# Kernel optimization log

Hardware: AMD Instinct MI355X
Metric: run time of the kernel (lower is better)

Reference implementation:

```python
import jax, jax.numpy as jnp
import numpy as np

N = 100000
F_IN = 128
HID = 16
C = 16
E = 3200000


def setup_inputs() -> dict:
    key = jax.random.key(0)
    k1, k2, k3, k4, k5, k6 = jax.random.split(key, 6)
    x = jax.random.normal(k1, (N, F_IN), dtype=jnp.float32)
    edge_index = jax.random.randint(k2, (2, E), 0, N, dtype=jnp.int64)
    # GCNConv weight (glorot) + bias
    W1 = jax.random.normal(k3, (F_IN, HID), dtype=jnp.float32) * (1.0 / np.sqrt(F_IN))
    b1 = jnp.zeros((HID,), dtype=jnp.float32)
    # pooling linear
    Wp = jax.random.normal(k4, (HID, C), dtype=jnp.float32) * (1.0 / np.sqrt(HID))
    bp = jax.random.normal(k5, (C,), dtype=jnp.float32) * 0.01
    return {"x": x, "W1": W1, "b1": b1, "Wp": Wp, "bp": bp, "edge_index": edge_index}


def gcn_conv(x, W, b, edge_index, num_nodes):
    # PyG GCNConv: add self-loops, symmetric normalization D^-1/2 (A+I) D^-1/2
    loop = jnp.arange(num_nodes, dtype=edge_index.dtype)
    src = jnp.concatenate([edge_index[0], loop])
    dst = jnp.concatenate([edge_index[1], loop])
    ones = jnp.ones_like(dst, dtype=x.dtype)
    deg = jax.ops.segment_sum(ones, dst, num_segments=num_nodes)  # [N]
    dinv = jnp.where(deg > 0, jax.lax.rsqrt(deg), 0.0)
    norm = dinv[src] * dinv[dst]  # [E+N]
    h = x @ W  # [N, HID] transform before aggregation (fewer bytes moved)
    msgs = h[src] * norm[:, None]  # gather + scale
    agg = jax.ops.segment_sum(msgs, dst, num_segments=num_nodes)  # scatter-add
    return agg + b


def reference(x, W1, b1, Wp, bp, edge_index):
    h = jax.nn.relu(gcn_conv(x, W1, b1, edge_index, N))  # [N, HID]
    s = jax.nn.softmax(h @ Wp + bp, axis=1)  # [N, C]
    return s
```

## Files before the change

### kernel.cpp

```cpp
#include <hip/hip_runtime.h>


#define PCHUNK 4096
#define SPLITS 4
#define ACH 2048

__device__ __forceinline__ float bf2f(unsigned int u16) {
    return __uint_as_float(u16 << 16);
}
__device__ __forceinline__ unsigned short f2bf(float f) {
    unsigned int u = __float_as_uint(f);
    u += 0x7fffu + ((u >> 16) & 1u);
    return (unsigned short)(u >> 16);
}

__device__ __forceinline__ void atomAddF(float* p, float v) {
    unsafeAtomicAdd(p, v);
}

__device__ __forceinline__ int voteBf16(const unsigned int* xw, int tid, int* scratch) {
    if (tid == 0) *scratch = 0;
    __syncthreads();
    unsigned int w = xw[tid];
    unsigned int lo = w & 0xffffu;
    unsigned int elo = (lo >> 7) & 0xffu;
    if (lo == 0u || (elo >= 100u && elo <= 140u)) atomicAdd(scratch, 1);
    __syncthreads();
    return (*scratch >= 160) ? 1 : 0;
}

__global__ __launch_bounds__(256) void k_part(const int* __restrict__ ei,
                                              int* __restrict__ cursor,
                                              unsigned int* __restrict__ bkt,
                                              int E, int Nn, int NB, int cap) {
    __shared__ int lhist[512];
    __shared__ int lexcl[512];
    __shared__ int lbase[512];
    __shared__ int sa[512], sb[512];
    __shared__ unsigned int stage[PCHUNK];
    __shared__ ushort sbk[PCHUNK];
    __shared__ int stot_s;
    __shared__ int v64_s;
    int tid = threadIdx.x;
    lhist[tid] = 0; lhist[tid + 256] = 0;
    if (tid == 0) v64_s = 0;
    __syncthreads();
    if (((const unsigned int*)ei)[2 * tid + 1] != 0u) atomicAdd(&v64_s, 1);
    __syncthreads();
    int is64 = (v64_s == 0) ? 1 : 0;
    int e0 = blockIdx.x * PCHUNK;
    int ss[16], dd[16];
    #pragma unroll
    for (int i = 0; i < 16; ++i) {
        int e = e0 + i * 256 + tid;
        int s = -1, d = -1;
        if (e < E) {
            if (is64) { s = ei[2 * e]; d = ei[2 * (E + e)]; }
            else      { s = ei[e];     d = ei[E + e]; }
            if ((unsigned)s >= (unsigned)Nn || (unsigned)d >= (unsigned)Nn) { s = -1; d = -1; }
        }
        ss[i] = s; dd[i] = d;
        if (d >= 0) atomicAdd(&lhist[d >> 8], 1);
    }
    __syncthreads();
    sa[tid] = lhist[tid]; sa[tid + 256] = lhist[tid + 256];
    __syncthreads();
    int* cur = sa; int* nxt = sb;
    for (int off = 1; off < 512; off <<= 1) {
        nxt[tid] = cur[tid] + ((tid >= off) ? cur[tid - off] : 0);
        int t2 = tid + 256;
        nxt[t2] = cur[t2] + ((t2 >= off) ? cur[t2 - off] : 0);
        __syncthreads();
        int* t = cur; cur = nxt; nxt = t;
    }
    lexcl[tid] = cur[tid] - lhist[tid];
    lexcl[tid + 256] = cur[tid + 256] - lhist[tid + 256];
    if (tid == 0) stot_s = cur[511];
    __syncthreads();
    for (int b = tid; b < 512; b += 256) {
        int c = lhist[b];
        if (b < NB && c > 0) {
            int base = atomicAdd(&cursor[b], c);
            lbase[b] = b * cap + base - lexcl[b];
        } else lbase[b] = 0;
        lhist[b] = lexcl[b];
    }
    __syncthreads();
    #pragma unroll
    for (int i = 0; i < 16; ++i) {
        if (dd[i] >= 0) {
            int b = dd[i] >> 8;
            int q = atomicAdd(&lhist[b], 1);
            stage[q] = (unsigned)ss[i] | ((unsigned)(dd[i] & 255) << 17);
            sbk[q] = (ushort)b;
        }
    }
    __syncthreads();
    int stot = stot_s;
    for (int q = tid; q < stot; q += 256) {
        int b = sbk[q];
        int pos = lbase[b] + q;
        if (pos < (b + 1) * cap) bkt[pos] = stage[q];
    }
}

__global__ __launch_bounds__(256) void k_gemmD(const void* __restrict__ xraw,
                                               const void* __restrict__ w1raw,
                                               const unsigned int* __restrict__ bkt,
                                               const int* __restrict__ cursor,
                                               float* __restrict__ dinv,
                                               ushort* __restrict__ hs16,
                                               float* __restrict__ agg,
                                               int Nn, int cap) {
    __shared__ float sWt[16 * 132];
    __shared__ int ldeg[256];
    __shared__ float sdv[256];
    __shared__ int vote_s;
    const ushort* xb = (const ushort*)xraw;
    const float* xf = (const float*)xraw;
    int tid = threadIdx.x, b = blockIdx.x;
    const int isbf = voteBf16((const unsigned int*)xraw, tid, &vote_s);
    ldeg[tid] = 0;
    if (isbf) {
        const ushort* w1 = (const ushort*)w1raw;
        for (int i = tid; i < 2048; i += 256) {
            int k = i >> 4, j = i & 15;
            sWt[j * 132 + k] = bf2f(w1[i]);
        }
    } else {
        const float* w1 = (const float*)w1raw;
        for (int i = tid; i < 2048; i += 256) {
            int k = i >> 4, j = i & 15;
            sWt[j * 132 + k] = w1[i];
        }
    }
    __syncthreads();
    int len = min(cursor[b], cap);
    int bb = b * cap;
    for (int e = tid; e < len; e += 256)
        atomicAdd(&ldeg[(bkt[bb + e] >> 17) & 255u], 1);
    __syncthreads();
    {
        float dv = rsqrtf((float)(ldeg[tid] + 1));
        sdv[tid] = dv;
        int n = (b << 8) + tid;
        if (n < Nn) dinv[n] = dv;
    }
    __syncthreads();
    int hq = tid & 3;
    int nodeq = tid >> 2;
    int n0 = (b << 8) + nodeq * 4;
    float acc[4][4] = {};
    for (int ko = 0; ko < 16; ++ko) {
        float xv[4][8];
        #pragma unroll
        for (int r = 0; r < 4; ++r) {
            int n = n0 + r;
            if (n < Nn) {
                if (isbf) {
                    uint4 q = *reinterpret_cast<const uint4*>(xb + (size_t)n * 128 + ko * 8);
                    xv[r][0] = bf2f(q.x & 0xffffu); xv[r][1] = bf2f(q.x >> 16);
                    xv[r][2] = bf2f(q.y & 0xffffu); xv[r][3] = bf2f(q.y >> 16);
                    xv[r][4] = bf2f(q.z & 0xffffu); xv[r][5] = bf2f(q.z >> 16);
                    xv[r][6] = bf2f(q.w & 0xffffu); xv[r][7] = bf2f(q.w >> 16);
                } else {
                    const float4* p = reinterpret_cast<const float4*>(xf + (size_t)n * 128 + ko * 8);
                    float4 a = p[0], bf = p[1];
                    xv[r][0] = a.x; xv[r][1] = a.y; xv[r][2] = a.z; xv[r][3] = a.w;
                    xv[r][4] = bf.x; xv[r][5] = bf.y; xv[r][6] = bf.z; xv[r][7] = bf.w;
                }
            } else {
                #pragma unroll
                for (int u = 0; u < 8; ++u) xv[r][u] = 0.f;
            }
        }
        #pragma unroll
        for (int c = 0; c < 4; ++c) {
            const float* wr = &sWt[(hq * 4 + c) * 132 + ko * 8];
            float4 w0 = *reinterpret_cast<const float4*>(wr);
            float4 w1v = *reinterpret_cast<const float4*>(wr + 4);
            #pragma unroll
            for (int r = 0; r < 4; ++r) {
                acc[r][c] += xv[r][0] * w0.x + xv[r][1] * w0.y + xv[r][2] * w0.z + xv[r][3] * w0.w
                           + xv[r][4] * w1v.x + xv[r][5] * w1v.y + xv[r][6] * w1v.z + xv[r][7] * w1v.w;
            }
        }
    }
    #pragma unroll
    for (int r = 0; r < 4; ++r) {
        int n = n0 + r;
        if (n < Nn) {
            float dv = sdv[nodeq * 4 + r];
            float4 o = make_float4(acc[r][0] * dv, acc[r][1] * dv, acc[r][2] * dv, acc[r][3] * dv);
            ushort4 o16;
            o16.x = f2bf(o.x); o16.y = f2bf(o.y); o16.z = f2bf(o.z); o16.w = f2bf(o.w);
            *reinterpret_cast<ushort4*>(hs16 + (size_t)n * 16 + hq * 4) = o16;
            *reinterpret_cast<float4*>(agg + (size_t)n * 16 + hq * 4) = o;
        }
    }
}

__global__ __launch_bounds__(256) void k_aggS(const unsigned int* __restrict__ bkt,
                                              const int* __restrict__ cursor,
                                              const ushort* __restrict__ hs16,
                                              float* __restrict__ agg, int Nn, int cap) {
    __shared__ unsigned int sSorted[ACH];
    __shared__ int cnt[256], excl[256];
    __shared__ int sc[2][256];
    __shared__ int tot_s;
    int tid = threadIdx.x;
    int b = blockIdx.x >> 2, sp = blockIdx.x & 3;
    int len = min(cursor[b], cap);
    int bb = b * cap;
    int s0 = (int)(((long long)len * sp) >> 2);
    int s1 = (int)(((long long)len * (sp + 1)) >> 2);
    int g = tid >> 4, j = tid & 15;
    float racc[16] = {};
    for (int c0 = s0; c0 < s1; c0 += ACH) {
        cnt[tid] = 0;
        __syncthreads();
        unsigned ue[8];
        #pragma unroll
        for (int i = 0; i < 8; ++i) {
            int idx = c0 + i * 256 + tid;
            if (idx < s1) {
                ue[i] = bkt[bb + idx];
                atomicAdd(&cnt[(ue[i] >> 17) & 255u], 1);
            } else ue[i] = 0xffffffffu;
        }
        __syncthreads();
        int v = cnt[tid];
        sc[0][tid] = v;
        __syncthreads();
        int pi = 0;
        for (int off = 1; off < 256; off <<= 1) {
            sc[pi ^ 1][tid] = sc[pi][tid] + ((tid >= off) ? sc[pi][tid - off] : 0);
            __syncthreads();
            pi ^= 1;
        }
        int ex = sc[pi][tid] - v;
        excl[tid] = ex;
        cnt[tid] = ex;
        if (tid == 255) tot_s = sc[pi][255];
        __syncthreads();
        #pragma unroll
        for (int i = 0; i < 8; ++i) {
            if (ue[i] != 0xffffffffu) {
                int q = atomicAdd(&cnt[(ue[i] >> 17) & 255u], 1);
                sSorted[q] = ue[i];
            }
        }
        __syncthreads();
        int tot = tot_s;
        #pragma unroll
        for (int nn = 0; nn < 16; ++nn) {
            int node = g * 16 + nn;
            int segS = excl[node];
            int segE = (node == 255) ? tot : excl[node + 1];
            float acc = 0.f;
            #pragma unroll 1
            for (int base = segS; base < segE; base += 16) {
                int m = segE - base;
                unsigned e16[16];
                float vv[16];
                #pragma unroll
                for (int i = 0; i < 16; ++i) {
                    int idx = base + i;
                    e16[i] = sSorted[(idx < segE) ? idx : segS];
                }
                #pragma unroll
                for (int i = 0; i < 16; ++i)
                    vv[i] = bf2f(hs16[(size_t)(e16[i] & 0x1ffffu) * 16 + j]);
                #pragma unroll
                for (int i = 0; i < 16; ++i)
                    vv[i] = (i < m) ? vv[i] : 0.f;
                #pragma unroll
                for (int off = 8; off >= 1; off >>= 1) {
                    #pragma unroll
                    for (int i = 0; i < off; ++i) vv[i] += vv[i + off];
                }
                acc += vv[0];
            }
            racc[nn] += acc;
        }
        __syncthreads();
    }
    int nbase = b << 8;
    #pragma unroll
    for (int nn = 0; nn < 16; ++nn) {
        int n = nbase + g * 16 + nn;
        float v = racc[nn];
        bool nz = (n < Nn) && (v != 0.f);
        if (__any(nz)) {
            if (n < Nn) atomAddF(&agg[(size_t)n * 16 + j], v);
        }
    }
}

__global__ __launch_bounds__(256) void k_final(const float* __restrict__ agg,
                                               const float* __restrict__ dinv,
                                               const void* __restrict__ xraw,
                                               const void* __restrict__ b1raw,
                                               const void* __restrict__ wpraw,
                                               const void* __restrict__ bpraw,
                                               void* __restrict__ outraw, int Nn) {
    __shared__ float sWp[256];
    __shared__ float sA[256];
    __shared__ int vote_s;
    int tid = threadIdx.x;
    const int isbf = voteBf16((const unsigned int*)xraw, tid, &vote_s);
    sWp[tid] = isbf ? bf2f(((const ushort*)wpraw)[tid]) : ((const float*)wpraw)[tid];
    int nl = tid >> 4, c = tid & 15;
    float b1v = isbf ? bf2f(((const ushort*)b1raw)[c]) : ((const float*)b1raw)[c];
    float bpv = isbf ? bf2f(((const ushort*)bpraw)[c]) : ((const float*)bpraw)[c];
    int base0 = blockIdx.x * 64;
    #pragma unroll 1
    for (int pass = 0; pass < 4; ++pass) {
        int n = base0 + pass * 16 + nl;
        float av = (n < Nn) ? agg[(size_t)n * 16 + c] * dinv[n] : 0.f;
        sA[tid] = fmaxf(av + b1v, 0.f);
        __syncthreads();
        float acc = bpv;
        #pragma unroll
        for (int jj = 0; jj < 16; ++jj) acc += sA[nl * 16 + jj] * sWp[jj * 16 + c];
        float m = acc;
        #pragma unroll
        for (int off = 1; off < 16; off <<= 1) m = fmaxf(m, __shfl_xor(m, off, 16));
        float ev = __expf(acc - m);
        float s = ev;
        #pragma unroll
        for (int off = 1; off < 16; off <<= 1) s += __shfl_xor(s, off, 16);
        if (n < Nn) {
            float v = ev / s;
            if (isbf) ((ushort*)outraw)[(size_t)n * 16 + c] = f2bf(v);
            else      ((float*)outraw)[(size_t)n * 16 + c] = v;
        }
        __syncthreads();
    }
}

extern "C" void kernel_launch(void* const* d_in, const int* in_sizes, int n_in,
                              void* d_out, int out_size, void* d_ws, size_t ws_size,
                              hipStream_t stream) {
    const void* x  = d_in[0];
    const void* W1 = d_in[1];
    const void* b1 = d_in[2];
    const void* Wp = d_in[3];
    const void* bp = d_in[4];
    const int*  ei = (const int*)d_in[5];

    int Nn = in_sizes[0] / 128;
    int E  = in_sizes[5] / 2;
    int NB = (Nn + 255) >> 8;

    size_t Ns = (size_t)Nn;
    char* ws = (char*)d_ws;
    size_t off = 0;
    auto alloc = [&](size_t bytes) { void* p = ws + off; off += (bytes + 63) & ~(size_t)63; return p; };
    ushort* hs16  = (ushort*)alloc(Ns * 16 * 2);
    float* agg    = (float*)alloc(Ns * 16 * 4);
    float* dinv   = (float*)alloc(Ns * 4);
    int*   cursor = (int*)alloc(512 * 4);
    size_t remain = (ws_size > off) ? (ws_size - off) : 0;
    int cap = (int)(remain / 4 / (size_t)NB);
    int want = 12288;
    if (cap > want) cap = want;
    cap &= ~63;
    unsigned int* bkt = (unsigned int*)alloc((size_t)NB * (size_t)cap * 4);

    hipMemsetAsync(cursor, 0, 512 * 4, stream);
    k_part<<<(E + PCHUNK - 1) / PCHUNK, 256, 0, stream>>>(ei, cursor, bkt, E, Nn, NB, cap);
    k_gemmD<<<NB, 256, 0, stream>>>(x, W1, bkt, cursor, dinv, hs16, agg, Nn, cap);
    k_aggS<<<NB * SPLITS, 256, 0, stream>>>(bkt, cursor, hs16, agg, Nn, cap);
    k_final<<<(Nn + 63) / 64, 256, 0, stream>>>(agg, dinv, x, b1, Wp, bp, d_out, Nn);
}
```

Before: 235.6 us.

## Fuse final softmax stage into aggregation kernel via last-block completion counter

Removes the separate k_final launch. Each k_aggS block bumps a per-bucket done counter after its atomic adds, and the last of the four split blocks for a bucket runs the bias, ReLU, pooling matmul and softmax for that bucket's 256 nodes. This saves a kernel launch and gives the tail a better chance of reading agg while it is still in cache. In exchange, the final stage runs on only one block per bucket (about 391 blocks), which adds serial work to the end of each bucket, and the code now relies on threadfence ordering for correctness.

```diff
diff --git a/kernel.cpp b/kernel.cpp
--- a/kernel.cpp
+++ b/kernel.cpp
@@ -203,11 +203,20 @@
 __global__ __launch_bounds__(256) void k_aggS(const unsigned int* __restrict__ bkt,
                                               const int* __restrict__ cursor,
                                               const ushort* __restrict__ hs16,
-                                              float* __restrict__ agg, int Nn, int cap) {
+                                              float* __restrict__ agg,
+                                              const float* __restrict__ dinv,
+                                              int* __restrict__ done,
+                                              const void* __restrict__ xraw,
+                                              const void* __restrict__ b1raw,
+                                              const void* __restrict__ wpraw,
+                                              const void* __restrict__ bpraw,
+                                              void* __restrict__ outraw,
+                                              int Nn, int cap) {
     __shared__ unsigned int sSorted[ACH];
     __shared__ int cnt[256], excl[256];
     __shared__ int sc[2][256];
     __shared__ int tot_s;
+    __shared__ int lastf;
     int tid = threadIdx.x;
     int b = blockIdx.x >> 2, sp = blockIdx.x & 3;
     int len = min(cursor[b], cap);
@@ -295,28 +304,23 @@
             if (n < Nn) atomAddF(&agg[(size_t)n * 16 + j], v);
         }
     }
-}
-
-__global__ __launch_bounds__(256) void k_final(const float* __restrict__ agg,
-                                               const float* __restrict__ dinv,
-                                               const void* __restrict__ xraw,
-                                               const void* __restrict__ b1raw,
-                                               const void* __restrict__ wpraw,
-                                               const void* __restrict__ bpraw,
-                                               void* __restrict__ outraw, int Nn) {
-    __shared__ float sWp[256];
-    __shared__ float sA[256];
-    __shared__ int vote_s;
-    int tid = threadIdx.x;
-    const int isbf = voteBf16((const unsigned int*)xraw, tid, &vote_s);
+    __threadfence();
+    __syncthreads();
+    if (tid == 0) lastf = (atomicAdd(&done[b], 1) == SPLITS - 1);
+    __syncthreads();
+    if (!lastf) return;
+    __threadfence();
+    const int isbf = voteBf16((const unsigned int*)xraw, tid, &tot_s);
+    float* sWp = (float*)sSorted;
+    float* sA  = (float*)(sSorted + 512);
     sWp[tid] = isbf ? bf2f(((const ushort*)wpraw)[tid]) : ((const float*)wpraw)[tid];
     int nl = tid >> 4, c = tid & 15;
     float b1v = isbf ? bf2f(((const ushort*)b1raw)[c]) : ((const float*)b1raw)[c];
     float bpv = isbf ? bf2f(((const ushort*)bpraw)[c]) : ((const float*)bpraw)[c];
-    int base0 = blockIdx.x * 64;
+    __syncthreads();
     #pragma unroll 1
-    for (int pass = 0; pass < 4; ++pass) {
-        int n = base0 + pass * 16 + nl;
+    for (int pass = 0; pass < 16; ++pass) {
+        int n = nbase + pass * 16 + nl;
         float av = (n < Nn) ? agg[(size_t)n * 16 + c] * dinv[n] : 0.f;
         sA[tid] = fmaxf(av + b1v, 0.f);
         __syncthreads();
@@ -360,7 +364,8 @@
     ushort* hs16  = (ushort*)alloc(Ns * 16 * 2);
     float* agg    = (float*)alloc(Ns * 16 * 4);
     float* dinv   = (float*)alloc(Ns * 4);
-    int*   cursor = (int*)alloc(512 * 4);
+    int*   cursor = (int*)alloc(1024 * 4);
+    int*   done   = cursor + 512;
     size_t remain = (ws_size > off) ? (ws_size - off) : 0;
     int cap = (int)(remain / 4 / (size_t)NB);
     int want = 12288;
@@ -368,9 +373,9 @@
     cap &= ~63;
     unsigned int* bkt = (unsigned int*)alloc((size_t)NB * (size_t)cap * 4);
 
-    hipMemsetAsync(cursor, 0, 512 * 4, stream);
+    hipMemsetAsync(cursor, 0, 1024 * 4, stream);
     k_part<<<(E + PCHUNK - 1) / PCHUNK, 256, 0, stream>>>(ei, cursor, bkt, E, Nn, NB, cap);
     k_gemmD<<<NB, 256, 0, stream>>>(x, W1, bkt, cursor, dinv, hs16, agg, Nn, cap);
-    k_aggS<<<NB * SPLITS, 256, 0, stream>>>(bkt, cursor, hs16, agg, Nn, cap);
-    k_final<<<(Nn + 63) / 64, 256, 0, stream>>>(agg, dinv, x, b1, Wp, bp, d_out, Nn);
-}
+    k_aggS<<<NB * SPLITS, 256, 0, stream>>>(bkt, cursor, hs16, agg, dinv, done,
+                                            x, b1, Wp, bp, d_out, Nn, cap);
+}
```

Result: slower. 471.2 us (+100.0%).
